# Optimization experiments

Hardware: AMD Instinct MI355X
Metric: run time of the kernel (lower is better)

## Reference

```python
import jax, jax.numpy as jnp
import numpy as np

B, S, H, HD = 2, 4096, 8, 64
D = H * HD
EPS = 1e-5

def setup_inputs() -> dict:
    key = jax.random.key(0)
    ks = jax.random.split(key, 8)
    sc = 0.05
    return {
        "x": jax.random.normal(ks[0], (B, S, D), jnp.float32),
        "y": jax.random.normal(ks[1], (B, S, D), jnp.float32),
        "Wk": jax.random.normal(ks[2], (H, HD, HD), jnp.float32) * sc,
        "bk": jax.random.normal(ks[3], (H, HD), jnp.float32) * sc,
        "Wq": jax.random.normal(ks[4], (H, HD, HD), jnp.float32) * sc,
        "bq": jax.random.normal(ks[5], (H, HD), jnp.float32) * sc,
        "Wv": jax.random.normal(ks[6], (H, HD, HD), jnp.float32) * sc,
        "bv": jax.random.normal(ks[7], (H, HD), jnp.float32) * sc,
        "gamma": jnp.ones((D,), jnp.float32),
        "beta": jnp.zeros((D,), jnp.float32),
    }

def reference(x, y, Wk, bk, Wq, bq, Wv, bv, gamma, beta):
    b, s, d = x.shape
    # slice-per-head == reshape to [B,S,H,HD]
    xh = x.reshape(b, s, H, HD)
    yh = y.reshape(b, s, H, HD)
    # per-head linear projections (batched over heads)
    K = jnp.einsum('bshd,hde->bshe', xh, Wk) + bk  # [B,S,H,HD]
    Q = jnp.einsum('bshd,hde->bshe', yh, Wq) + bq
    V = jnp.einsum('bshd,hde->bshe', xh, Wv) + bv
    scale = 1.0 / jnp.sqrt(jnp.float32(HD))
    scores = jnp.einsum('bshe,bthe->bhst', Q, K) * scale  # [B,H,S,S]
    attn = jax.nn.softmax(scores, axis=-1)
    out = jnp.einsum('bhst,bthe->bshe', attn, V)  # [B,S,H,HD]
    out = out.reshape(b, s, d) + y
    # LayerNorm over last dim
    mu = jnp.mean(out, axis=-1, keepdims=True)
    var = jnp.mean(jnp.square(out - mu), axis=-1, keepdims=True)
    return (out - mu) * jax.lax.rsqrt(var + EPS) * gamma + beta
```

## Files before the change

### kernel.cpp

```cpp
#include <hip/hip_runtime.h>
#include <hip/hip_bf16.h>

#define B_  2
#define S_  4096
#define H_  8
#define HD_ 64
#define D_  512
#define NSPLIT 2
#define NT_ ((S_ / NSPLIT) / 64)

using bf16x8 = __attribute__((ext_vector_type(8))) short;
using f32x4  = __attribute__((ext_vector_type(4))) float;
using f32x16 = __attribute__((ext_vector_type(16))) float;
using u32x4  = __attribute__((ext_vector_type(4))) unsigned int;

__device__ __forceinline__ unsigned short f2bf(float f) {
    unsigned int u = __float_as_uint(f);
    u += 0x7FFFu + ((u >> 16) & 1u);
    return (unsigned short)(u >> 16);
}

__device__ __forceinline__ float bf2f(short s) {
    return __uint_as_float(((unsigned int)(unsigned short)s) << 16);
}

__device__ __forceinline__ unsigned int pkbf(float a, float b) {
    unsigned int r;
    asm("v_cvt_pk_bf16_f32 %0, %1, %2" : "=v"(r) : "v"(a), "v"(b));
    return r;
}

__device__ __forceinline__ float ex2(float x) {
    float r;
    asm("v_exp_f32 %0, %1" : "=v"(r) : "v"(x));
    return r;
}

__device__ __forceinline__ void gl16(const unsigned short* g, unsigned short* l) {
    __builtin_amdgcn_global_load_lds(
        (const __attribute__((address_space(1))) unsigned int*)g,
        (__attribute__((address_space(3))) unsigned int*)l, 16, 0, 0);
}

__global__ __launch_bounds__(256) void proj_kernel(
    const float* __restrict__ x,  const float* __restrict__ yy,
    const float* __restrict__ Wk, const float* __restrict__ bk,
    const float* __restrict__ Wq, const float* __restrict__ bq,
    const float* __restrict__ Wv, const float* __restrict__ bv,
    unsigned short* __restrict__ Qw, unsigned short* __restrict__ Kw,
    unsigned short* __restrict__ Vt)
{
    __shared__ __attribute__((aligned(16))) unsigned short xs[64][72];
    __shared__ __attribute__((aligned(16))) unsigned short ys[64][72];
    __shared__ __attribute__((aligned(16))) unsigned short wtk[64][72];
    __shared__ __attribute__((aligned(16))) unsigned short wtq[64][72];
    __shared__ __attribute__((aligned(16))) unsigned short wtv[64][72];
    __shared__ __attribute__((aligned(16))) unsigned short vtl[64][72];

    const int t  = threadIdx.x;
    const int s0 = blockIdx.x * 64;
    const int bh = blockIdx.y;
    const int b  = bh >> 3, h = bh & 7;

    #pragma unroll
    for (int i = 0; i < 4; ++i) {
        int id = t + 256 * i;
        int row = id >> 4, c4 = id & 15;
        size_t ga = ((size_t)(b * S_ + s0 + row)) * D_ + h * HD_ + c4 * 4;
        float4 xv = *(const float4*)(x + ga);
        float4 yv = *(const float4*)(yy + ga);
        unsigned int xl = f2bf(xv.x) | ((unsigned int)f2bf(xv.y) << 16);
        unsigned int xh = f2bf(xv.z) | ((unsigned int)f2bf(xv.w) << 16);
        unsigned int yl = f2bf(yv.x) | ((unsigned int)f2bf(yv.y) << 16);
        unsigned int yh = f2bf(yv.z) | ((unsigned int)f2bf(yv.w) << 16);
        *(uint2*)&xs[row][c4 * 4] = make_uint2(xl, xh);
        *(uint2*)&ys[row][c4 * 4] = make_uint2(yl, yh);
    }
    #pragma unroll
    for (int i = 0; i < 4; ++i) {
        int id = t + 256 * i;
        int dd = id >> 4, e4 = id & 15;
        size_t wa = (size_t)(h * HD_ + dd) * HD_ + e4 * 4;
        float4 wk4 = *(const float4*)(Wk + wa);
        float4 wq4 = *(const float4*)(Wq + wa);
        float4 wv4 = *(const float4*)(Wv + wa);
        wtk[e4*4+0][dd] = f2bf(wk4.x); wtk[e4*4+1][dd] = f2bf(wk4.y);
        wtk[e4*4+2][dd] = f2bf(wk4.z); wtk[e4*4+3][dd] = f2bf(wk4.w);
        wtq[e4*4+0][dd] = f2bf(wq4.x); wtq[e4*4+1][dd] = f2bf(wq4.y);
        wtq[e4*4+2][dd] = f2bf(wq4.z); wtq[e4*4+3][dd] = f2bf(wq4.w);
        wtv[e4*4+0][dd] = f2bf(wv4.x); wtv[e4*4+1][dd] = f2bf(wv4.y);
        wtv[e4*4+2][dd] = f2bf(wv4.z); wtv[e4*4+3][dd] = f2bf(wv4.w);
    }
    __syncthreads();

    const int lane = t & 63, w = t >> 6;
    const int g = lane >> 4, lq = lane & 15;

    bf16x8 ax[2], ay[2];
    #pragma unroll
    for (int kk = 0; kk < 2; ++kk) {
        ax[kk] = *(const bf16x8*)&xs[w*16 + lq][kk*32 + g*8];
        ay[kk] = *(const bf16x8*)&ys[w*16 + lq][kk*32 + g*8];
    }

    f32x4 ak[4], aq[4], av[4];
    #pragma unroll
    for (int n = 0; n < 4; ++n) { ak[n] = (f32x4)0.f; aq[n] = (f32x4)0.f; av[n] = (f32x4)0.f; }

    #pragma unroll
    for (int n = 0; n < 4; ++n) {
        #pragma unroll
        for (int kk = 0; kk < 2; ++kk) {
            bf16x8 bk_ = *(const bf16x8*)&wtk[n*16 + lq][kk*32 + g*8];
            ak[n] = __builtin_amdgcn_mfma_f32_16x16x32_bf16(ax[kk], bk_, ak[n], 0, 0, 0);
            bf16x8 bq_ = *(const bf16x8*)&wtq[n*16 + lq][kk*32 + g*8];
            aq[n] = __builtin_amdgcn_mfma_f32_16x16x32_bf16(ay[kk], bq_, aq[n], 0, 0, 0);
            bf16x8 bv_ = *(const bf16x8*)&wtv[n*16 + lq][kk*32 + g*8];
            av[n] = __builtin_amdgcn_mfma_f32_16x16x32_bf16(ax[kk], bv_, av[n], 0, 0, 0);
        }
    }

    const float cscale = 0.125f * 1.44269504088896340736f;
    #pragma unroll
    for (int n = 0; n < 4; ++n) {
        int e = n*16 + lq;
        float bkv = bk[h*HD_ + e], bqv = bq[h*HD_ + e], bvv = bv[h*HD_ + e];
        #pragma unroll
        for (int r = 0; r < 4; ++r) {
            int srow = w*16 + g*4 + r;
            size_t o = ((size_t)bh * S_ + s0 + srow) * HD_ + e;
            Kw[o] = f2bf(ak[n][r] + bkv);
            Qw[o] = f2bf((aq[n][r] + bqv) * cscale);
            vtl[e][srow] = f2bf(av[n][r] + bvv);
        }
    }
    __syncthreads();
    #pragma unroll
    for (int i = 0; i < 2; ++i) {
        int id = t + 256 * i;
        int e = id >> 3, c = id & 7;
        bf16x8 v = *(const bf16x8*)&vtl[e][c*8];
        *(bf16x8*)(Vt + ((size_t)bh * HD_ + e) * S_ + s0 + c*8) = v;
    }
}

__global__ __launch_bounds__(256, 4) void attn_kernel(
    const unsigned short* __restrict__ Qw, const unsigned short* __restrict__ Kw,
    const unsigned short* __restrict__ Vt, unsigned short* __restrict__ U,
    float* __restrict__ sbuf)
{
    __shared__ __attribute__((aligned(16))) unsigned short ksh[2][64][64];
    __shared__ __attribute__((aligned(16))) unsigned short vsh[2][64][64];

    const int t = threadIdx.x, lane = t & 63, w = t >> 6;
    const int lx = lane & 31, hi = lane >> 5;
    const int q0 = blockIdx.x * 128;
    const int bh = blockIdx.y;
    const int z  = blockIdx.z;
    const int b  = bh >> 3, h = bh & 7;
    const int kvbase = z * (S_ / NSPLIT);

    const unsigned short* Kb = Kw + ((size_t)bh * S_ + kvbase) * HD_;
    const unsigned short* Vb = Vt + (size_t)bh * HD_ * S_ + kvbase;

    bf16x8 qf[4];
    #pragma unroll
    for (int kq = 0; kq < 4; ++kq)
        qf[kq] = *(const bf16x8*)(Qw + ((size_t)bh*S_ + q0 + w*32 + lx)*HD_ + kq*16 + hi*8);

    f32x16 oaccT[2];
    oaccT[0] = (f32x16)0.f; oaccT[1] = (f32x16)0.f;
    float ssum = 0.f;

    const int w16 = w * 16;
    const int sw8 = ((lane & 7) ^ (lane >> 3)) * 8;
    const unsigned short* kg0 = Kb + (size_t)(w16 +     (lane >> 3)) * HD_ + sw8;
    const unsigned short* kg1 = Kb + (size_t)(w16 + 8 + (lane >> 3)) * HD_ + sw8;
    const unsigned short* vg0 = Vb + (size_t)(w16 +     (lane >> 3)) * S_  + sw8;
    const unsigned short* vg1 = Vb + (size_t)(w16 + 8 + (lane >> 3)) * S_  + sw8;

    gl16(kg0, &ksh[0][w16][0]);     gl16(kg1, &ksh[0][w16 + 8][0]);
    gl16(vg0, &vsh[0][w16][0]);     gl16(vg1, &vsh[0][w16 + 8][0]);
    kg0 += 64 * HD_; kg1 += 64 * HD_; vg0 += 64; vg1 += 64;
    __syncthreads();

#define TILE(CUR, KT)                                                         \
    {                                                                         \
        if ((KT) + 1 < NT_) {                                                 \
            gl16(kg0, &ksh[(CUR)^1][w16][0]);                                 \
            gl16(kg1, &ksh[(CUR)^1][w16 + 8][0]);                             \
            gl16(vg0, &vsh[(CUR)^1][w16][0]);                                 \
            gl16(vg1, &vsh[(CUR)^1][w16 + 8][0]);                             \
            kg0 += 64 * HD_; kg1 += 64 * HD_; vg0 += 64; vg1 += 64;           \
        }                                                                     \
        __builtin_amdgcn_s_setprio(1);                                        \
        f32x16 st0 = (f32x16)0.f, st1 = (f32x16)0.f;                          \
        _Pragma("unroll")                                                     \
        for (int kq = 0; kq < 4; ++kq) {                                      \
            bf16x8 kf0 = *(const bf16x8*)&ksh[CUR][lx][(kq*16 + hi*8) ^ ((lx & 7)*8)]; \
            st0 = __builtin_amdgcn_mfma_f32_32x32x16_bf16(kf0, qf[kq], st0, 0, 0, 0);  \
            bf16x8 kf1 = *(const bf16x8*)&ksh[CUR][32 + lx][(kq*16 + hi*8) ^ ((lx & 7)*8)]; \
            st1 = __builtin_amdgcn_mfma_f32_32x32x16_bf16(kf1, qf[kq], st1, 0, 0, 0);  \
        }                                                                     \
        float ts = 0.f;                                                       \
        _Pragma("unroll")                                                     \
        for (int r = 0; r < 16; ++r) {                                        \
            st0[r] = ex2(st0[r]); st1[r] = ex2(st1[r]);                       \
            ts += st0[r]; ts += st1[r];                                       \
        }                                                                     \
        ssum += ts;                                                           \
        _Pragma("unroll")                                                     \
        for (int ks = 0; ks < 4; ++ks) {                                      \
            const int u0 = (ks & 1) * 2;                                      \
            unsigned int w0, w1, w2, w3;                                      \
            if (ks < 2) {                                                     \
                w0 = pkbf(st0[4*u0+0],     st0[4*u0+1]);                      \
                w2 = pkbf(st0[4*(u0+1)+0], st0[4*(u0+1)+1]);                  \
                w1 = pkbf(st0[4*u0+2],     st0[4*u0+3]);                      \
                w3 = pkbf(st0[4*(u0+1)+2], st0[4*(u0+1)+3]);                  \
            } else {                                                          \
                w0 = pkbf(st1[4*u0+0],     st1[4*u0+1]);                      \
                w2 = pkbf(st1[4*(u0+1)+0], st1[4*(u0+1)+1]);                  \
                w1 = pkbf(st1[4*u0+2],     st1[4*u0+3]);                      \
                w3 = pkbf(st1[4*(u0+1)+2], st1[4*(u0+1)+3]);                  \
            }                                                                 \
            asm("v_permlane32_swap_b32 %0, %1" : "+v"(w0), "+v"(w2));         \
            asm("v_permlane32_swap_b32 %0, %1" : "+v"(w1), "+v"(w3));         \
            u32x4 pw; pw.x = w0; pw.y = w1; pw.z = w2; pw.w = w3;             \
            bf16x8 pB = __builtin_bit_cast(bf16x8, pw);                       \
            _Pragma("unroll")                                                 \
            for (int d0 = 0; d0 < 2; ++d0) {                                  \
                const int vrow = d0*32 + lx;                                  \
                bf16x8 vf = *(const bf16x8*)&vsh[CUR][vrow][(ks*16 + hi*8) ^ ((vrow & 7)*8)]; \
                oaccT[d0] = __builtin_amdgcn_mfma_f32_32x32x16_bf16(vf, pB, oaccT[d0], 0, 0, 0); \
            }                                                                 \
        }                                                                     \
        __builtin_amdgcn_s_setprio(0);                                        \
        __syncthreads();                                                      \
    }

    for (int kt = 0; kt < NT_; kt += 2) {
        TILE(0, kt)
        TILE(1, kt + 1)
    }
#undef TILE

    ssum += __shfl_xor(ssum, 32);
    unsigned short* osh = &ksh[0][0][0] + w * (32 * 64);
    #pragma unroll
    for (int d0 = 0; d0 < 2; ++d0)
        #pragma unroll
        for (int u = 0; u < 4; ++u) {
            unsigned int lo = pkbf(oaccT[d0][4*u+0], oaccT[d0][4*u+1]);
            unsigned int hw = pkbf(oaccT[d0][4*u+2], oaccT[d0][4*u+3]);
            int d = d0*32 + 8*u + 4*hi;
            *(uint2*)&osh[lx*64 + (d ^ ((lx & 7)*8))] = make_uint2(lo, hw);
        }
    __syncthreads();
    {
        const int rloc = lane >> 3;
        const int dcol = (lane & 7) * 8;
        unsigned short* ubase = U + (size_t)z * (B_*S_*(size_t)D_)
                                  + ((size_t)b * S_ + q0 + w*32) * D_ + h * HD_;
        #pragma unroll
        for (int i = 0; i < 4; ++i) {
            int q = i*8 + rloc;
            bf16x8 ov = *(const bf16x8*)&osh[q*64 + (dcol ^ ((q & 7)*8))];
            *(bf16x8*)(ubase + (size_t)q * D_ + dcol) = ov;
        }
    }
    if (hi == 0) {
        const int qrow = q0 + w*32 + lx;
        sbuf[(size_t)z * (B_*S_*H_) + ((size_t)b * S_ + qrow) * H_ + h] = ssum;
    }
}

__global__ __launch_bounds__(256) void ln_kernel(
    const unsigned short* __restrict__ U, const float* __restrict__ sbuf,
    const float* __restrict__ yy,
    const float* __restrict__ gamma, const float* __restrict__ beta,
    float* __restrict__ out)
{
    const int t = threadIdx.x, lane = t & 63, w = t >> 6;
    const size_t row = (size_t)blockIdx.x * 4 + w;
    const int h = lane >> 3;

    float s0 = sbuf[row * H_ + h];
    float s1 = sbuf[(size_t)(B_*S_)*H_ + row * H_ + h];
    float inv = 1.0f / (s0 + s1);

    bf16x8 u0 = *(const bf16x8*)(U + row * D_ + lane*8);
    bf16x8 u1 = *(const bf16x8*)(U + (size_t)(B_*S_)*(size_t)D_ + row * D_ + lane*8);
    const float* yr = yy + row * D_;

    float v[8];
    #pragma unroll
    for (int i = 0; i < 2; ++i) {
        float4 yv = *(const float4*)(yr + lane*8 + i*4);
        v[i*4+0] = (bf2f(u0[i*4+0]) + bf2f(u1[i*4+0]))*inv + yv.x;
        v[i*4+1] = (bf2f(u0[i*4+1]) + bf2f(u1[i*4+1]))*inv + yv.y;
        v[i*4+2] = (bf2f(u0[i*4+2]) + bf2f(u1[i*4+2]))*inv + yv.z;
        v[i*4+3] = (bf2f(u0[i*4+3]) + bf2f(u1[i*4+3]))*inv + yv.w;
    }
    float s = 0.f;
    #pragma unroll
    for (int j = 0; j < 8; ++j) s += v[j];
    #pragma unroll
    for (int o = 32; o >= 1; o >>= 1) s += __shfl_xor(s, o);
    float mu = s * (1.f / 512.f);
    float qs = 0.f;
    #pragma unroll
    for (int j = 0; j < 8; ++j) { float d = v[j] - mu; qs += d * d; }
    #pragma unroll
    for (int o = 32; o >= 1; o >>= 1) qs += __shfl_xor(qs, o);
    float rstd = rsqrtf(qs * (1.f / 512.f) + 1e-5f);

    #pragma unroll
    for (int i = 0; i < 2; ++i) {
        float4 gm = *(const float4*)(gamma + lane*8 + i*4);
        float4 bt = *(const float4*)(beta  + lane*8 + i*4);
        float4 o4;
        o4.x = (v[i*4+0] - mu) * rstd * gm.x + bt.x;
        o4.y = (v[i*4+1] - mu) * rstd * gm.y + bt.y;
        o4.z = (v[i*4+2] - mu) * rstd * gm.z + bt.z;
        o4.w = (v[i*4+3] - mu) * rstd * gm.w + bt.w;
        *(float4*)(out + row * D_ + lane*8 + i*4) = o4;
    }
}

extern "C" void kernel_launch(void* const* d_in, const int* in_sizes, int n_in,
                              void* d_out, int out_size, void* d_ws, size_t ws_size,
                              hipStream_t stream) {
    const float* x     = (const float*)d_in[0];
    const float* y     = (const float*)d_in[1];
    const float* Wk    = (const float*)d_in[2];
    const float* bk    = (const float*)d_in[3];
    const float* Wq    = (const float*)d_in[4];
    const float* bq    = (const float*)d_in[5];
    const float* Wv    = (const float*)d_in[6];
    const float* bv    = (const float*)d_in[7];
    const float* gamma = (const float*)d_in[8];
    const float* beta  = (const float*)d_in[9];

    const size_t NTOK = (size_t)B_ * H_ * S_ * HD_;
    unsigned short* Qw = (unsigned short*)d_ws;
    unsigned short* Kw = Qw + NTOK;
    unsigned short* Vt = Kw + NTOK;
    unsigned short* U  = Vt + NTOK;
    float* sbuf = (float*)(U + (size_t)NSPLIT * B_ * S_ * D_);

    dim3 pgrid(S_ / 64, B_ * H_);
    proj_kernel<<<pgrid, 256, 0, stream>>>(x, y, Wk, bk, Wq, bq, Wv, bv, Qw, Kw, Vt);
    dim3 agrid(S_ / 128, B_ * H_, NSPLIT);
    attn_kernel<<<agrid, 256, 0, stream>>>(Qw, Kw, Vt, U, sbuf);
    ln_kernel<<<(B_ * S_) / 4, 256, 0, stream>>>(U, sbuf, y, gamma, beta, (float*)d_out);
}
```

Measured before the change: 102.2 us.

## Software-pipeline attention loop: overlap QK of next tile with PV of previous

Restructures the attention inner loop so that each iteration computes QK^T for tile k while running the PV MFMAs for tile k-1 using previously packed probabilities. V is triple-buffered in LDS so the previous tile's V stays resident while the next one is staged. A prologue and epilogue handle the pipeline fill and drain. The aim is to hide the exp and pack latency behind MFMA work, at the cost of more LDS, more live registers, and hardcoded trip counts for NT=32.

After: 200.7 us. +96.4%, slower.

```diff
diff --git a/kernel.cpp b/kernel.cpp
--- a/kernel.cpp
+++ b/kernel.cpp
@@ -150,7 +150,7 @@
     float* __restrict__ sbuf)
 {
     __shared__ __attribute__((aligned(16))) unsigned short ksh[2][64][64];
-    __shared__ __attribute__((aligned(16))) unsigned short vsh[2][64][64];
+    __shared__ __attribute__((aligned(16))) unsigned short vsh[3][64][64];
 
     const int t = threadIdx.x, lane = t & 63, w = t >> 6;
     const int lx = lane & 31, hi = lane >> 5;
@@ -170,7 +170,8 @@
 
     f32x16 oaccT[2];
     oaccT[0] = (f32x16)0.f; oaccT[1] = (f32x16)0.f;
-    float ssum = 0.f;
+    float ssA = 0.f, ssB = 0.f;
+    u32x4 pw0, pw1, pw2, pw3;
 
     const int w16 = w * 16;
     const int sw8 = ((lane & 7) ^ (lane >> 3)) * 8;
@@ -184,67 +185,102 @@
     kg0 += 64 * HD_; kg1 += 64 * HD_; vg0 += 64; vg1 += 64;
     __syncthreads();
 
-#define TILE(CUR, KT)                                                         \
-    {                                                                         \
-        if ((KT) + 1 < NT_) {                                                 \
-            gl16(kg0, &ksh[(CUR)^1][w16][0]);                                 \
-            gl16(kg1, &ksh[(CUR)^1][w16 + 8][0]);                             \
-            gl16(vg0, &vsh[(CUR)^1][w16][0]);                                 \
-            gl16(vg1, &vsh[(CUR)^1][w16 + 8][0]);                             \
-            kg0 += 64 * HD_; kg1 += 64 * HD_; vg0 += 64; vg1 += 64;           \
-        }                                                                     \
-        __builtin_amdgcn_s_setprio(1);                                        \
+#define QK(KB)                                                                \
         f32x16 st0 = (f32x16)0.f, st1 = (f32x16)0.f;                          \
         _Pragma("unroll")                                                     \
         for (int kq = 0; kq < 4; ++kq) {                                      \
-            bf16x8 kf0 = *(const bf16x8*)&ksh[CUR][lx][(kq*16 + hi*8) ^ ((lx & 7)*8)]; \
-            st0 = __builtin_amdgcn_mfma_f32_32x32x16_bf16(kf0, qf[kq], st0, 0, 0, 0);  \
-            bf16x8 kf1 = *(const bf16x8*)&ksh[CUR][32 + lx][(kq*16 + hi*8) ^ ((lx & 7)*8)]; \
-            st1 = __builtin_amdgcn_mfma_f32_32x32x16_bf16(kf1, qf[kq], st1, 0, 0, 0);  \
-        }                                                                     \
-        float ts = 0.f;                                                       \
-        _Pragma("unroll")                                                     \
-        for (int r = 0; r < 16; ++r) {                                        \
-            st0[r] = ex2(st0[r]); st1[r] = ex2(st1[r]);                       \
-            ts += st0[r]; ts += st1[r];                                       \
-        }                                                                     \
-        ssum += ts;                                                           \
+            bf16x8 kf0 = *(const bf16x8*)&ksh[KB][lx][(kq*16 + hi*8) ^ ((lx & 7)*8)]; \
+            st0 = __builtin_amdgcn_mfma_f32_32x32x16_bf16(kf0, qf[kq], st0, 0, 0, 0); \
+            bf16x8 kf1 = *(const bf16x8*)&ksh[KB][32 + lx][(kq*16 + hi*8) ^ ((lx & 7)*8)]; \
+            st1 = __builtin_amdgcn_mfma_f32_32x32x16_bf16(kf1, qf[kq], st1, 0, 0, 0); \
+        }
+
+#define PV(VPB)                                                               \
         _Pragma("unroll")                                                     \
         for (int ks = 0; ks < 4; ++ks) {                                      \
-            const int u0 = (ks & 1) * 2;                                      \
-            unsigned int w0, w1, w2, w3;                                      \
-            if (ks < 2) {                                                     \
-                w0 = pkbf(st0[4*u0+0],     st0[4*u0+1]);                      \
-                w2 = pkbf(st0[4*(u0+1)+0], st0[4*(u0+1)+1]);                  \
-                w1 = pkbf(st0[4*u0+2],     st0[4*u0+3]);                      \
-                w3 = pkbf(st0[4*(u0+1)+2], st0[4*(u0+1)+3]);                  \
-            } else {                                                          \
-                w0 = pkbf(st1[4*u0+0],     st1[4*u0+1]);                      \
-                w2 = pkbf(st1[4*(u0+1)+0], st1[4*(u0+1)+1]);                  \
-                w1 = pkbf(st1[4*u0+2],     st1[4*u0+3]);                      \
-                w3 = pkbf(st1[4*(u0+1)+2], st1[4*(u0+1)+3]);                  \
-            }                                                                 \
-            asm("v_permlane32_swap_b32 %0, %1" : "+v"(w0), "+v"(w2));         \
-            asm("v_permlane32_swap_b32 %0, %1" : "+v"(w1), "+v"(w3));         \
-            u32x4 pw; pw.x = w0; pw.y = w1; pw.z = w2; pw.w = w3;             \
-            bf16x8 pB = __builtin_bit_cast(bf16x8, pw);                       \
+            u32x4 pws = (ks == 0) ? pw0 : (ks == 1) ? pw1 : (ks == 2) ? pw2 : pw3; \
+            bf16x8 pB = __builtin_bit_cast(bf16x8, pws);                      \
             _Pragma("unroll")                                                 \
             for (int d0 = 0; d0 < 2; ++d0) {                                  \
-                const int vrow = d0*32 + lx;                                  \
-                bf16x8 vf = *(const bf16x8*)&vsh[CUR][vrow][(ks*16 + hi*8) ^ ((vrow & 7)*8)]; \
+                bf16x8 vf = *(const bf16x8*)&vsh[VPB][d0*32 + lx][(ks*16 + hi*8) ^ ((lx & 7)*8)]; \
                 oaccT[d0] = __builtin_amdgcn_mfma_f32_32x32x16_bf16(vf, pB, oaccT[d0], 0, 0, 0); \
             }                                                                 \
-        }                                                                     \
+        }
+
+#define SM()                                                                  \
+        {                                                                     \
+            float ta = 0.f, tb = 0.f;                                         \
+            _Pragma("unroll")                                                 \
+            for (int r = 0; r < 16; ++r) {                                    \
+                st0[r] = ex2(st0[r]); st1[r] = ex2(st1[r]);                   \
+                ta += st0[r]; tb += st1[r];                                   \
+            }                                                                 \
+            ssA += ta; ssB += tb;                                             \
+            _Pragma("unroll")                                                 \
+            for (int ks = 0; ks < 4; ++ks) {                                  \
+                const int u0 = (ks & 1) * 2;                                  \
+                unsigned int a0, a1, a2, a3;                                  \
+                if (ks < 2) {                                                 \
+                    a0 = pkbf(st0[4*u0+0],     st0[4*u0+1]);                  \
+                    a2 = pkbf(st0[4*(u0+1)+0], st0[4*(u0+1)+1]);              \
+                    a1 = pkbf(st0[4*u0+2],     st0[4*u0+3]);                  \
+                    a3 = pkbf(st0[4*(u0+1)+2], st0[4*(u0+1)+3]);              \
+                } else {                                                      \
+                    a0 = pkbf(st1[4*u0+0],     st1[4*u0+1]);                  \
+                    a2 = pkbf(st1[4*(u0+1)+0], st1[4*(u0+1)+1]);              \
+                    a1 = pkbf(st1[4*u0+2],     st1[4*u0+3]);                  \
+                    a3 = pkbf(st1[4*(u0+1)+2], st1[4*(u0+1)+3]);              \
+                }                                                             \
+                asm("v_permlane32_swap_b32 %0, %1" : "+v"(a0), "+v"(a2));     \
+                asm("v_permlane32_swap_b32 %0, %1" : "+v"(a1), "+v"(a3));     \
+                u32x4 pn; pn.x = a0; pn.y = a1; pn.z = a2; pn.w = a3;         \
+                if (ks == 0) pw0 = pn; else if (ks == 1) pw1 = pn;            \
+                else if (ks == 2) pw2 = pn; else pw3 = pn;                    \
+            }                                                                 \
+        }
+
+#define STAGE(KB2, VB2)                                                       \
+        gl16(kg0, &ksh[KB2][w16][0]);     gl16(kg1, &ksh[KB2][w16 + 8][0]);   \
+        gl16(vg0, &vsh[VB2][w16][0]);     gl16(vg1, &vsh[VB2][w16 + 8][0]);   \
+        kg0 += 64 * HD_; kg1 += 64 * HD_; vg0 += 64; vg1 += 64;
+
+#define TILE(STG, KB, VB, VPB)                                                \
+    {                                                                         \
+        if (STG) { STAGE((KB)^1, ((VB)+1)%3) }                                \
+        __builtin_amdgcn_s_setprio(1);                                        \
+        QK(KB)                                                                \
+        PV(VPB)                                                               \
+        SM()                                                                  \
         __builtin_amdgcn_s_setprio(0);                                        \
         __syncthreads();                                                      \
     }
 
-    for (int kt = 0; kt < NT_; kt += 2) {
-        TILE(0, kt)
-        TILE(1, kt + 1)
-    }
+    {
+        STAGE(1, 1)
+        __builtin_amdgcn_s_setprio(1);
+        QK(0)
+        SM()
+        __builtin_amdgcn_s_setprio(0);
+        __syncthreads();
+    }
+    for (int kt = 1; kt + 5 <= 30; kt += 6) {
+        TILE(1, 1, 1, 0)
+        TILE(1, 0, 2, 1)
+        TILE(1, 1, 0, 2)
+        TILE(1, 0, 1, 0)
+        TILE(1, 1, 2, 1)
+        TILE(1, 0, 0, 2)
+    }
+    TILE(0, 1, 1, 0)
+    PV(1)
+
 #undef TILE
-
+#undef STAGE
+#undef SM
+#undef PV
+#undef QK
+
+    float ssum = ssA + ssB;
     ssum += __shfl_xor(ssum, 32);
     unsigned short* osh = &ksh[0][0][0] + w * (32 * 64);
     #pragma unroll
```
